# Optimization experiments

Measured on AMD Instinct MI355X. Metric: run time of the kernel, lower is better.

The kernel has to match this reference:

```python
import jax, jax.numpy as jnp
import numpy as np

H, C = 8, 32          # heads, per-head channels (h_feats)
NEG_SLOPE = 0.2


def setup_inputs() -> dict:
    key = jax.random.key(0)
    ks = jax.random.split(key, 9)
    N, E, F_IN, F_E = 50000, 800000, 128, 16
    x = jax.random.normal(ks[0], (N, F_IN), jnp.float32)
    edge_index = jax.random.randint(ks[1], (2, E), 0, N, jnp.int64)
    edge_attr = jax.random.normal(ks[2], (E, F_E), jnp.float32)
    s = 1.0 / np.sqrt(F_IN)
    W = jax.random.normal(ks[3], (H * C, F_IN), jnp.float32) * s
    W_edge = jax.random.normal(ks[4], (H * C, F_E), jnp.float32) * (1.0 / np.sqrt(F_E))
    att_src = jax.random.normal(ks[5], (H, C), jnp.float32) * (1.0 / np.sqrt(C))
    att_dst = jax.random.normal(ks[6], (H, C), jnp.float32) * (1.0 / np.sqrt(C))
    att_edge = jax.random.normal(ks[7], (H, C), jnp.float32) * (1.0 / np.sqrt(C))
    bias = jnp.zeros((C,), jnp.float32)
    return {"x": x, "edge_index": edge_index, "edge_attr": edge_attr,
            "W": W, "W_edge": W_edge, "att_src": att_src, "att_dst": att_dst,
            "att_edge": att_edge, "bias": bias}


def reference(x, edge_index, edge_attr, W, W_edge, att_src, att_dst, att_edge, bias):
    N = x.shape[0]
    src, dst = edge_index[0], edge_index[1]

    # --- add self loops, edge_attr fill_value='mean' (per-dst mean of incoming attrs) ---
    deg = jax.ops.segment_sum(jnp.ones_like(dst, dtype=edge_attr.dtype), dst, num_segments=N)
    loop_attr = jax.ops.segment_sum(edge_attr, dst, num_segments=N) / jnp.maximum(deg, 1.0)[:, None]
    loop = jnp.arange(N, dtype=src.dtype)
    src = jnp.concatenate([src, loop])
    dst = jnp.concatenate([dst, loop])
    ea = jnp.concatenate([edge_attr, loop_attr], axis=0)  # [E+N, F_e]

    # --- node projection and per-node attention terms ---
    xh = (x @ W.T).reshape(N, H, C)                      # [N,H,C]
    a_src = jnp.einsum('nhc,hc->nh', xh, att_src)        # [N,H]
    a_dst = jnp.einsum('nhc,hc->nh', xh, att_dst)        # [N,H]

    # edge attention folded: (lin_edge(e).view(E,H,C) * att_edge).sum(-1) == e @ M
    M = jnp.einsum('hcf,hc->fh', W_edge.reshape(H, C, -1), att_edge)  # [F_e,H]
    a_edge = ea @ M                                      # [E+N,H]

    alpha = a_src[src] + a_dst[dst] + a_edge             # [E+N,H]
    alpha = jnp.where(alpha >= 0, alpha, NEG_SLOPE * alpha)

    # --- scatter-softmax over edges grouped by dst node ---
    amax = jax.ops.segment_max(alpha, dst, num_segments=N)  # every node has a self loop
    ex = jnp.exp(alpha - amax[dst])
    denom = jax.ops.segment_sum(ex, dst, num_segments=N)
    att = ex / denom[dst]                                # [E+N,H]

    # --- weighted message scatter-sum ---
    msg = xh[src] * att[..., None]                       # [E+N,H,C]
    out = jax.ops.segment_sum(msg, dst, num_segments=N)  # [N,H,C]
    return out.mean(axis=1) + bias                       # concat=False -> head mean
```

## Files before the change

kernel.cpp:

```cpp
#include <hip/hip_runtime.h>
#include <math.h>

#define H 8
#define C 32
#define HC 256
#define FE 16
#define FIN 128
#define NEG_SLOPE 0.2f

__device__ __forceinline__ unsigned short f2bf(float f) {
  union { float f; unsigned int u; } a; a.f = f;
  unsigned int r = a.u;
  unsigned int lsb = (r >> 16) & 1u;
  r += 0x7fffu + lsb;
  return (unsigned short)(r >> 16);
}
__device__ __forceinline__ float bf2f(unsigned short s) {
  union { unsigned int u; float f; } a; a.u = ((unsigned int)s) << 16;
  return a.f;
}

__global__ void k_M(const float* __restrict__ W_edge, const float* __restrict__ att_edge,
                    float* __restrict__ M) {
  int t = threadIdx.x;
  int f = t >> 3, h = t & 7;
  float acc = 0.f;
#pragma unroll
  for (int c = 0; c < C; ++c)
    acc += W_edge[(h * C + c) * FE + f] * att_edge[h * C + c];
  M[f * H + h] = acc;
}

__global__ __launch_bounds__(256) void k_xh(const float* __restrict__ x,
                                            const float* __restrict__ W,
                                            const float* __restrict__ att_src,
                                            const float* __restrict__ att_dst,
                                            unsigned short* __restrict__ xhb,
                                            float* __restrict__ a_src,
                                            float* __restrict__ a_dst, int N) {
  __shared__ float As[16][132];
  __shared__ float Bs[16][132];
  int t = threadIdx.x;
  int rg = t >> 4;
  int cg = t & 15;
  int rb = blockIdx.x * 128;
  int cb = blockIdx.y * 128;
  int lr = t >> 2;
  int lk = (t & 3) * 4;

  float acc[8][8] = {};
  for (int k0 = 0; k0 < FIN; k0 += 16) {
#pragma unroll
    for (int half = 0; half < 2; ++half) {
      int row = half * 64 + lr;
      float4 va = make_float4(0.f, 0.f, 0.f, 0.f);
      if (rb + row < N) va = *(const float4*)&x[(size_t)(rb + row) * FIN + k0 + lk];
      As[lk + 0][row] = va.x; As[lk + 1][row] = va.y; As[lk + 2][row] = va.z; As[lk + 3][row] = va.w;
      float4 vb = *(const float4*)&W[(size_t)(cb + row) * FIN + k0 + lk];
      Bs[lk + 0][row] = vb.x; Bs[lk + 1][row] = vb.y; Bs[lk + 2][row] = vb.z; Bs[lk + 3][row] = vb.w;
    }
    __syncthreads();
#pragma unroll
    for (int k = 0; k < 16; ++k) {
      float4 a0 = *(const float4*)&As[k][rg * 8];
      float4 a1 = *(const float4*)&As[k][rg * 8 + 4];
      float4 b0 = *(const float4*)&Bs[k][cg * 8];
      float4 b1 = *(const float4*)&Bs[k][cg * 8 + 4];
      float av[8] = {a0.x, a0.y, a0.z, a0.w, a1.x, a1.y, a1.z, a1.w};
      float bv[8] = {b0.x, b0.y, b0.z, b0.w, b1.x, b1.y, b1.z, b1.w};
#pragma unroll
      for (int i = 0; i < 8; ++i)
#pragma unroll
        for (int j = 0; j < 8; ++j) acc[i][j] = fmaf(av[i], bv[j], acc[i][j]);
    }
    __syncthreads();
  }

  float asv[8], adv[8];
#pragma unroll
  for (int j = 0; j < 8; ++j) {
    asv[j] = att_src[cb + cg * 8 + j];
    adv[j] = att_dst[cb + cg * 8 + j];
  }
  int head = blockIdx.y * 4 + (cg >> 2);
#pragma unroll
  for (int i = 0; i < 8; ++i) {
    int r = rb + rg * 8 + i;
    if (r >= N) continue;
    unsigned int p0 = (unsigned int)f2bf(acc[i][0]) | ((unsigned int)f2bf(acc[i][1]) << 16);
    unsigned int p1 = (unsigned int)f2bf(acc[i][2]) | ((unsigned int)f2bf(acc[i][3]) << 16);
    unsigned int p2 = (unsigned int)f2bf(acc[i][4]) | ((unsigned int)f2bf(acc[i][5]) << 16);
    unsigned int p3 = (unsigned int)f2bf(acc[i][6]) | ((unsigned int)f2bf(acc[i][7]) << 16);
    uint4 pk = make_uint4(p0, p1, p2, p3);
    *(uint4*)&xhb[(size_t)r * HC + cb + cg * 8] = pk;
    float ps = 0.f, pd = 0.f;
#pragma unroll
    for (int j = 0; j < 8; ++j) { ps = fmaf(acc[i][j], asv[j], ps); pd = fmaf(acc[i][j], adv[j], pd); }
    ps += __shfl_xor(ps, 1, 64); ps += __shfl_xor(ps, 2, 64);
    pd += __shfl_xor(pd, 1, 64); pd += __shfl_xor(pd, 2, 64);
    if ((t & 3) == 0) {
      a_src[r * H + head] = ps;
      a_dst[r * H + head] = pd;
    }
  }
}

__global__ __launch_bounds__(256) void k_deg(const int* __restrict__ ei,
                                             int* __restrict__ deg, int E) {
  int e = blockIdx.x * 256 + threadIdx.x;
  if (e < E) atomicAdd(&deg[ei[E + e]], 1);
}

__global__ __launch_bounds__(256) void k_scan1(const int* __restrict__ deg,
                                               int* __restrict__ bsum, int N) {
  int t = threadIdx.x;
  int i = blockIdx.x * 256 + t;
  int v = (i < N) ? deg[i] : 0;
#pragma unroll
  for (int m = 1; m < 64; m <<= 1) v += __shfl_xor(v, m, 64);
  __shared__ int wsum[4];
  if ((t & 63) == 0) wsum[t >> 6] = v;
  __syncthreads();
  if (t == 0) bsum[blockIdx.x] = wsum[0] + wsum[1] + wsum[2] + wsum[3];
}

__global__ __launch_bounds__(256) void k_scan2(const int* __restrict__ bsum,
                                               int* __restrict__ boff, int nb) {
  __shared__ int buf[256];
  int t = threadIdx.x;
  int v = (t < nb) ? bsum[t] : 0;
  buf[t] = v;
  __syncthreads();
  for (int off = 1; off < 256; off <<= 1) {
    int y = (t >= off) ? buf[t - off] : 0;
    __syncthreads();
    buf[t] += y;
    __syncthreads();
  }
  if (t < nb) boff[t] = buf[t] - v;
}

__global__ __launch_bounds__(256) void k_scan3(const int* __restrict__ deg,
                                               const int* __restrict__ boff,
                                               int* __restrict__ rowptr,
                                               int* __restrict__ wo, int N, int E) {
  __shared__ int buf[256];
  int t = threadIdx.x;
  int i = blockIdx.x * 256 + t;
  int v = (i < N) ? deg[i] : 0;
  buf[t] = v;
  __syncthreads();
  for (int off = 1; off < 256; off <<= 1) {
    int y = (t >= off) ? buf[t - off] : 0;
    __syncthreads();
    buf[t] += y;
    __syncthreads();
  }
  if (i < N) {
    int ex = boff[blockIdx.x] + buf[t] - v;
    rowptr[i] = ex;
    wo[i] = ex;
  }
  if (i == 0) rowptr[N] = E;
}

__global__ __launch_bounds__(256) void k_edge_scatter(const int* __restrict__ ei,
                                                      const float* __restrict__ ea,
                                                      const float* __restrict__ M,
                                                      int* __restrict__ wo,
                                                      int* __restrict__ colsrc,
                                                      float* __restrict__ apre, int E) {
  __shared__ float Ms[FE * H];
  int t = threadIdx.x;
  if (t < FE * H) Ms[t] = M[t];
  __syncthreads();
  int e = blockIdx.x * 256 + t;
  if (e >= E) return;
  int s = ei[e], d = ei[E + e];
  const float4* p = (const float4*)&ea[(size_t)e * FE];
  float4 v0 = p[0], v1 = p[1], v2 = p[2], v3 = p[3];
  float eav[FE] = {v0.x, v0.y, v0.z, v0.w, v1.x, v1.y, v1.z, v1.w,
                   v2.x, v2.y, v2.z, v2.w, v3.x, v3.y, v3.z, v3.w};
  float o[H];
#pragma unroll
  for (int h = 0; h < H; ++h) {
    float acc = 0.f;
#pragma unroll
    for (int f = 0; f < FE; ++f) acc += eav[f] * Ms[f * H + h];
    o[h] = acc;
  }
  int pos = atomicAdd(&wo[d], 1);
  colsrc[pos] = s;
  float4* q = (float4*)&apre[(size_t)pos * H];
  q[0] = make_float4(o[0], o[1], o[2], o[3]);
  q[1] = make_float4(o[4], o[5], o[6], o[7]);
}

__global__ __launch_bounds__(256) void k_node(const unsigned short* __restrict__ xhb,
                                              const float* __restrict__ a_src,
                                              const float* __restrict__ a_dst,
                                              const float* __restrict__ apre,
                                              const int* __restrict__ colsrc,
                                              const int* __restrict__ rowptr,
                                              const float* __restrict__ bias,
                                              float* __restrict__ out, int N) {
  int lane = threadIdx.x & 63;
  int n = blockIdx.x * 4 + (threadIdx.x >> 6);
  if (n >= N) return;
  int start = rowptr[n];
  int deg = rowptr[n + 1] - start;
  int hc = lane >> 3;
  float adst = a_dst[n * H + hc];
  float asrc = a_src[n * H + hc];

  float m = -1e30f, l = 0.f, psum = 0.f;
  float ax = 0.f, ay = 0.f, az = 0.f, aw = 0.f;

#pragma unroll 4
  for (int j = 0; j < deg; ++j) {
    int src = colsrc[start + j];
    float ae = apre[(size_t)(start + j) * H + hc];
    psum += ae;
    float al = a_src[src * H + hc] + adst + ae;
    al = (al >= 0.f) ? al : NEG_SLOPE * al;
    float nm = fmaxf(m, al);
    float s = __expf(m - nm);
    float w = __expf(al - nm);
    m = nm;
    l = fmaf(l, s, w);
    ushort4 u = *(const ushort4*)&xhb[(size_t)src * HC + lane * 4];
    ax = fmaf(ax, s, w * bf2f(u.x));
    ay = fmaf(ay, s, w * bf2f(u.y));
    az = fmaf(az, s, w * bf2f(u.z));
    aw = fmaf(aw, s, w * bf2f(u.w));
  }

  float aself = asrc + adst + psum / fmaxf((float)deg, 1.f);
  aself = (aself >= 0.f) ? aself : NEG_SLOPE * aself;
  {
    float nm = fmaxf(m, aself);
    float s = __expf(m - nm);
    float w = __expf(aself - nm);
    m = nm;
    l = fmaf(l, s, w);
    ushort4 u = *(const ushort4*)&xhb[(size_t)n * HC + lane * 4];
    ax = fmaf(ax, s, w * bf2f(u.x));
    ay = fmaf(ay, s, w * bf2f(u.y));
    az = fmaf(az, s, w * bf2f(u.z));
    aw = fmaf(aw, s, w * bf2f(u.w));
  }
  float inv = 1.f / l;
  ax *= inv; ay *= inv; az *= inv; aw *= inv;

#pragma unroll
  for (int mm = 8; mm <= 32; mm <<= 1) {
    ax += __shfl_xor(ax, mm, 64);
    ay += __shfl_xor(ay, mm, 64);
    az += __shfl_xor(az, mm, 64);
    aw += __shfl_xor(aw, mm, 64);
  }
  if (lane < 8) {
    float4 b = ((const float4*)bias)[lane];
    float4 o;
    o.x = ax * 0.125f + b.x;
    o.y = ay * 0.125f + b.y;
    o.z = az * 0.125f + b.z;
    o.w = aw * 0.125f + b.w;
    ((float4*)&out[(size_t)n * C])[lane] = o;
  }
}

extern "C" void kernel_launch(void* const* d_in, const int* in_sizes, int n_in,
                              void* d_out, int out_size, void* d_ws, size_t ws_size,
                              hipStream_t stream) {
  const float* x        = (const float*)d_in[0];
  const int*   ei       = (const int*)d_in[1];
  const float* ea       = (const float*)d_in[2];
  const float* W        = (const float*)d_in[3];
  const float* W_edge   = (const float*)d_in[4];
  const float* att_src  = (const float*)d_in[5];
  const float* att_dst  = (const float*)d_in[6];
  const float* att_edge = (const float*)d_in[7];
  const float* bias     = (const float*)d_in[8];
  float* out = (float*)d_out;

  int N = in_sizes[0] / FIN;
  int E = in_sizes[1] / 2;
  int nb = (N + 255) / 256;

  char* ws = (char*)d_ws;
  auto take = [&](size_t bytes) {
    char* p = ws;
    ws += (bytes + 255) & ~(size_t)255;
    return p;
  };
  unsigned short* xhb = (unsigned short*)take((size_t)N * HC * 2);
  float* a_src  = (float*)take((size_t)N * H * 4);
  float* a_dst  = (float*)take((size_t)N * H * 4);
  float* apre   = (float*)take((size_t)E * H * 4);
  float* Mbuf   = (float*)take(FE * H * 4);
  int*   deg    = (int*)take((size_t)N * 4);
  int*   rowptr = (int*)take((size_t)(N + 1) * 4);
  int*   wo     = (int*)take((size_t)N * 4);
  int*   colsrc = (int*)take((size_t)E * 4);
  int*   bsum   = (int*)take((size_t)nb * 4);
  int*   boff   = (int*)take((size_t)nb * 4);

  hipMemsetAsync(deg, 0, (size_t)N * 4, stream);
  k_M<<<1, 128, 0, stream>>>(W_edge, att_edge, Mbuf);
  k_deg<<<(E + 255) / 256, 256, 0, stream>>>(ei, deg, E);
  k_xh<<<dim3((N + 127) / 128, HC / 128), 256, 0, stream>>>(x, W, att_src, att_dst, xhb, a_src, a_dst, N);
  k_scan1<<<nb, 256, 0, stream>>>(deg, bsum, N);
  k_scan2<<<1, 256, 0, stream>>>(bsum, boff, nb);
  k_scan3<<<nb, 256, 0, stream>>>(deg, boff, rowptr, wo, N, E);
  k_edge_scatter<<<(E + 255) / 256, 256, 0, stream>>>(ei, ea, Mbuf, wo, colsrc, apre, E);
  k_node<<<(N + 3) / 4, 256, 0, stream>>>(xhb, a_src, a_dst, apre, colsrc, rowptr, bias, out, N);
}
```

Before: 344.8 us.

## Use bf16 MFMA split-precision GEMM, rank-based CSR fill, bf16 edge logits

The node projection GEMM is rewritten to use MFMA 16x16x32 bf16 instructions, with the fp32 inputs split into hi/lo bf16 parts (three MFMAs per tile) to keep near-fp32 accuracy. Operands now load straight from global memory, with no LDS staging. The degree kernel records each edge's rank from its atomic, so the scatter kernel computes positions without a second round of atomics. The edge attention logits are stored as bf16 to halve that traffic, and the M matrix is computed inside the scatter kernel, which removes one launch. The costs are extra MFMA work, uncoalesced W/x loads, and precision loss in the edge logits.

```diff
diff --git a/kernel.cpp b/kernel.cpp
--- a/kernel.cpp
+++ b/kernel.cpp
@@ -8,27 +8,28 @@
 #define FIN 128
 #define NEG_SLOPE 0.2f
 
+typedef __attribute__((ext_vector_type(8))) short bf16x8;
+typedef __attribute__((ext_vector_type(4))) float f32x4;
+
 __device__ __forceinline__ unsigned short f2bf(float f) {
-  union { float f; unsigned int u; } a; a.f = f;
-  unsigned int r = a.u;
-  unsigned int lsb = (r >> 16) & 1u;
-  r += 0x7fffu + lsb;
-  return (unsigned short)(r >> 16);
+  unsigned int u = __float_as_uint(f);
+  unsigned int lsb = (u >> 16) & 1u;
+  u += 0x7fffu + lsb;
+  return (unsigned short)(u >> 16);
 }
 __device__ __forceinline__ float bf2f(unsigned short s) {
-  union { unsigned int u; float f; } a; a.u = ((unsigned int)s) << 16;
-  return a.f;
-}
-
-__global__ void k_M(const float* __restrict__ W_edge, const float* __restrict__ att_edge,
-                    float* __restrict__ M) {
-  int t = threadIdx.x;
-  int f = t >> 3, h = t & 7;
-  float acc = 0.f;
-#pragma unroll
-  for (int c = 0; c < C; ++c)
-    acc += W_edge[(h * C + c) * FE + f] * att_edge[h * C + c];
-  M[f * H + h] = acc;
+  return __uint_as_float(((unsigned int)s) << 16);
+}
+
+__device__ __forceinline__ void split8(const float* v, bf16x8& hi, bf16x8& lo) {
+#pragma unroll
+  for (int i = 0; i < 8; ++i) {
+    unsigned int u = __float_as_uint(v[i]);
+    unsigned int hu = u & 0xffff0000u;
+    float r = v[i] - __uint_as_float(hu);
+    hi[i] = (short)(hu >> 16);
+    lo[i] = (short)f2bf(r);
+  }
 }
 
 __global__ __launch_bounds__(256) void k_xh(const float* __restrict__ x,
@@ -38,77 +39,101 @@
                                             unsigned short* __restrict__ xhb,
                                             float* __restrict__ a_src,
                                             float* __restrict__ a_dst, int N) {
-  __shared__ float As[16][132];
-  __shared__ float Bs[16][132];
-  int t = threadIdx.x;
-  int rg = t >> 4;
-  int cg = t & 15;
-  int rb = blockIdx.x * 128;
-  int cb = blockIdx.y * 128;
-  int lr = t >> 2;
-  int lk = (t & 3) * 4;
-
-  float acc[8][8] = {};
-  for (int k0 = 0; k0 < FIN; k0 += 16) {
-#pragma unroll
-    for (int half = 0; half < 2; ++half) {
-      int row = half * 64 + lr;
-      float4 va = make_float4(0.f, 0.f, 0.f, 0.f);
-      if (rb + row < N) va = *(const float4*)&x[(size_t)(rb + row) * FIN + k0 + lk];
-      As[lk + 0][row] = va.x; As[lk + 1][row] = va.y; As[lk + 2][row] = va.z; As[lk + 3][row] = va.w;
-      float4 vb = *(const float4*)&W[(size_t)(cb + row) * FIN + k0 + lk];
-      Bs[lk + 0][row] = vb.x; Bs[lk + 1][row] = vb.y; Bs[lk + 2][row] = vb.z; Bs[lk + 3][row] = vb.w;
-    }
-    __syncthreads();
-#pragma unroll
-    for (int k = 0; k < 16; ++k) {
-      float4 a0 = *(const float4*)&As[k][rg * 8];
-      float4 a1 = *(const float4*)&As[k][rg * 8 + 4];
-      float4 b0 = *(const float4*)&Bs[k][cg * 8];
-      float4 b1 = *(const float4*)&Bs[k][cg * 8 + 4];
-      float av[8] = {a0.x, a0.y, a0.z, a0.w, a1.x, a1.y, a1.z, a1.w};
-      float bv[8] = {b0.x, b0.y, b0.z, b0.w, b1.x, b1.y, b1.z, b1.w};
-#pragma unroll
-      for (int i = 0; i < 8; ++i)
-#pragma unroll
-        for (int j = 0; j < 8; ++j) acc[i][j] = fmaf(av[i], bv[j], acc[i][j]);
-    }
-    __syncthreads();
-  }
-
-  float asv[8], adv[8];
-#pragma unroll
-  for (int j = 0; j < 8; ++j) {
-    asv[j] = att_src[cb + cg * 8 + j];
-    adv[j] = att_dst[cb + cg * 8 + j];
-  }
-  int head = blockIdx.y * 4 + (cg >> 2);
-#pragma unroll
-  for (int i = 0; i < 8; ++i) {
-    int r = rb + rg * 8 + i;
-    if (r >= N) continue;
-    unsigned int p0 = (unsigned int)f2bf(acc[i][0]) | ((unsigned int)f2bf(acc[i][1]) << 16);
-    unsigned int p1 = (unsigned int)f2bf(acc[i][2]) | ((unsigned int)f2bf(acc[i][3]) << 16);
-    unsigned int p2 = (unsigned int)f2bf(acc[i][4]) | ((unsigned int)f2bf(acc[i][5]) << 16);
-    unsigned int p3 = (unsigned int)f2bf(acc[i][6]) | ((unsigned int)f2bf(acc[i][7]) << 16);
-    uint4 pk = make_uint4(p0, p1, p2, p3);
-    *(uint4*)&xhb[(size_t)r * HC + cb + cg * 8] = pk;
-    float ps = 0.f, pd = 0.f;
-#pragma unroll
-    for (int j = 0; j < 8; ++j) { ps = fmaf(acc[i][j], asv[j], ps); pd = fmaf(acc[i][j], adv[j], pd); }
-    ps += __shfl_xor(ps, 1, 64); ps += __shfl_xor(ps, 2, 64);
-    pd += __shfl_xor(pd, 1, 64); pd += __shfl_xor(pd, 2, 64);
-    if ((t & 3) == 0) {
-      a_src[r * H + head] = ps;
-      a_dst[r * H + head] = pd;
+  int t = threadIdx.x;
+  int w = t >> 6, lane = t & 63;
+  int n15 = lane & 15, q = lane >> 4;
+  int nodeBase = blockIdx.x * 128 + w * 32;
+  int chBase = blockIdx.y * 128;
+
+  f32x4 acc[8][2];
+#pragma unroll
+  for (int mt = 0; mt < 8; ++mt)
+#pragma unroll
+    for (int nt = 0; nt < 2; ++nt) acc[mt][nt] = (f32x4)(0.f);
+
+  for (int ks = 0; ks < 4; ++ks) {
+    int kOff = ks * 32 + q * 8;
+    bf16x8 Bhi[2], Blo[2];
+#pragma unroll
+    for (int nt = 0; nt < 2; ++nt) {
+      int node = nodeBase + nt * 16 + n15;
+      int rn = (node < N) ? node : (N - 1);
+      const float* px = &x[(size_t)rn * FIN + kOff];
+      float vb[8];
+      *(float4*)&vb[0] = *(const float4*)px;
+      *(float4*)&vb[4] = *(const float4*)(px + 4);
+      split8(vb, Bhi[nt], Blo[nt]);
+    }
+#pragma unroll
+    for (int mt = 0; mt < 8; ++mt) {
+      const float* pw = &W[(size_t)(chBase + mt * 16 + n15) * FIN + kOff];
+      float va[8];
+      *(float4*)&va[0] = *(const float4*)pw;
+      *(float4*)&va[4] = *(const float4*)(pw + 4);
+      bf16x8 Ahi, Alo;
+      split8(va, Ahi, Alo);
+#pragma unroll
+      for (int nt = 0; nt < 2; ++nt) {
+        acc[mt][nt] = __builtin_amdgcn_mfma_f32_16x16x32_bf16(Ahi, Bhi[nt], acc[mt][nt], 0, 0, 0);
+        acc[mt][nt] = __builtin_amdgcn_mfma_f32_16x16x32_bf16(Ahi, Blo[nt], acc[mt][nt], 0, 0, 0);
+        acc[mt][nt] = __builtin_amdgcn_mfma_f32_16x16x32_bf16(Alo, Bhi[nt], acc[mt][nt], 0, 0, 0);
+      }
+    }
+  }
+
+  float ps[2][4] = {{0.f,0.f,0.f,0.f},{0.f,0.f,0.f,0.f}};
+  float pd[2][4] = {{0.f,0.f,0.f,0.f},{0.f,0.f,0.f,0.f}};
+#pragma unroll
+  for (int mt = 0; mt < 8; ++mt) {
+    int hl = mt >> 1;
+#pragma unroll
+    for (int r = 0; r < 4; ++r) {
+      int ch = chBase + mt * 16 + q * 4 + r;
+      float as_c = att_src[ch], ad_c = att_dst[ch];
+#pragma unroll
+      for (int nt = 0; nt < 2; ++nt) {
+        float val = acc[mt][nt][r];
+        ps[nt][hl] = fmaf(val, as_c, ps[nt][hl]);
+        pd[nt][hl] = fmaf(val, ad_c, pd[nt][hl]);
+      }
+    }
+#pragma unroll
+    for (int nt = 0; nt < 2; ++nt) {
+      int node = nodeBase + nt * 16 + n15;
+      if (node < N) {
+        ushort4 us;
+        us.x = f2bf(acc[mt][nt][0]); us.y = f2bf(acc[mt][nt][1]);
+        us.z = f2bf(acc[mt][nt][2]); us.w = f2bf(acc[mt][nt][3]);
+        *(ushort4*)&xhb[(size_t)node * HC + chBase + mt * 16 + q * 4] = us;
+      }
+    }
+  }
+#pragma unroll
+  for (int nt = 0; nt < 2; ++nt)
+#pragma unroll
+    for (int hl = 0; hl < 4; ++hl) {
+      ps[nt][hl] += __shfl_xor(ps[nt][hl], 16, 64);
+      ps[nt][hl] += __shfl_xor(ps[nt][hl], 32, 64);
+      pd[nt][hl] += __shfl_xor(pd[nt][hl], 16, 64);
+      pd[nt][hl] += __shfl_xor(pd[nt][hl], 32, 64);
+    }
+  if (q == 0) {
+#pragma unroll
+    for (int nt = 0; nt < 2; ++nt) {
+      int node = nodeBase + nt * 16 + n15;
+      if (node < N) {
+        *(float4*)&a_src[node * H + blockIdx.y * 4] = make_float4(ps[nt][0], ps[nt][1], ps[nt][2], ps[nt][3]);
+        *(float4*)&a_dst[node * H + blockIdx.y * 4] = make_float4(pd[nt][0], pd[nt][1], pd[nt][2], pd[nt][3]);
+      }
     }
   }
 }
 
 __global__ __launch_bounds__(256) void k_deg(const int* __restrict__ ei,
-                                             int* __restrict__ deg, int E) {
+                                             int* __restrict__ deg,
+                                             int* __restrict__ rank, int E) {
   int e = blockIdx.x * 256 + threadIdx.x;
-  if (e < E) atomicAdd(&deg[ei[E + e]], 1);
+  if (e < E) rank[e] = atomicAdd(&deg[ei[E + e]], 1);
 }
 
 __global__ __launch_bounds__(256) void k_scan1(const int* __restrict__ deg,
@@ -142,8 +167,7 @@
 
 __global__ __launch_bounds__(256) void k_scan3(const int* __restrict__ deg,
                                                const int* __restrict__ boff,
-                                               int* __restrict__ rowptr,
-                                               int* __restrict__ wo, int N, int E) {
+                                               int* __restrict__ rowptr, int N, int E) {
   __shared__ int buf[256];
   int t = threadIdx.x;
   int i = blockIdx.x * 256 + t;
@@ -156,23 +180,28 @@
     buf[t] += y;
     __syncthreads();
   }
-  if (i < N) {
-    int ex = boff[blockIdx.x] + buf[t] - v;
-    rowptr[i] = ex;
-    wo[i] = ex;
-  }
+  if (i < N) rowptr[i] = boff[blockIdx.x] + buf[t] - v;
   if (i == 0) rowptr[N] = E;
 }
 
 __global__ __launch_bounds__(256) void k_edge_scatter(const int* __restrict__ ei,
                                                       const float* __restrict__ ea,
-                                                      const float* __restrict__ M,
-                                                      int* __restrict__ wo,
+                                                      const float* __restrict__ W_edge,
+                                                      const float* __restrict__ att_edge,
+                                                      const int* __restrict__ rowptr,
+                                                      const int* __restrict__ rank,
                                                       int* __restrict__ colsrc,
-                                                      float* __restrict__ apre, int E) {
+                                                      unsigned short* __restrict__ apre16, int E) {
   __shared__ float Ms[FE * H];
   int t = threadIdx.x;
-  if (t < FE * H) Ms[t] = M[t];
+  if (t < FE * H) {
+    int f = t >> 3, h = t & 7;
+    float acc = 0.f;
+#pragma unroll
+    for (int c = 0; c < C; ++c)
+      acc += W_edge[(h * C + c) * FE + f] * att_edge[h * C + c];
+    Ms[f * H + h] = acc;
+  }
   __syncthreads();
   int e = blockIdx.x * 256 + t;
   if (e >= E) return;
@@ -189,17 +218,20 @@
     for (int f = 0; f < FE; ++f) acc += eav[f] * Ms[f * H + h];
     o[h] = acc;
   }
-  int pos = atomicAdd(&wo[d], 1);
+  int pos = rowptr[d] + rank[e];
   colsrc[pos] = s;
-  float4* q = (float4*)&apre[(size_t)pos * H];
-  q[0] = make_float4(o[0], o[1], o[2], o[3]);
-  q[1] = make_float4(o[4], o[5], o[6], o[7]);
+  uint4 pk;
+  pk.x = (unsigned int)f2bf(o[0]) | ((unsigned int)f2bf(o[1]) << 16);
+  pk.y = (unsigned int)f2bf(o[2]) | ((unsigned int)f2bf(o[3]) << 16);
+  pk.z = (unsigned int)f2bf(o[4]) | ((unsigned int)f2bf(o[5]) << 16);
+  pk.w = (unsigned int)f2bf(o[6]) | ((unsigned int)f2bf(o[7]) << 16);
+  *(uint4*)&apre16[(size_t)pos * H] = pk;
 }
 
 __global__ __launch_bounds__(256) void k_node(const unsigned short* __restrict__ xhb,
                                               const float* __restrict__ a_src,
                                               const float* __restrict__ a_dst,
-                                              const float* __restrict__ apre,
+                                              const unsigned short* __restrict__ apre16,
                                               const int* __restrict__ colsrc,
                                               const int* __restrict__ rowptr,
                                               const float* __restrict__ bias,
@@ -219,7 +251,7 @@
 #pragma unroll 4
   for (int j = 0; j < deg; ++j) {
     int src = colsrc[start + j];
-    float ae = apre[(size_t)(start + j) * H + hc];
+    float ae = bf2f(apre16[(size_t)(start + j) * H + hc]);
     psum += ae;
     float al = a_src[src * H + hc] + adst + ae;
     al = (al >= 0.f) ? al : NEG_SLOPE * al;
@@ -294,25 +326,23 @@
     ws += (bytes + 255) & ~(size_t)255;
     return p;
   };
-  unsigned short* xhb = (unsigned short*)take((size_t)N * HC * 2);
-  float* a_src  = (float*)take((size_t)N * H * 4);
-  float* a_dst  = (float*)take((size_t)N * H * 4);
-  float* apre   = (float*)take((size_t)E * H * 4);
-  float* Mbuf   = (float*)take(FE * H * 4);
-  int*   deg    = (int*)take((size_t)N * 4);
-  int*   rowptr = (int*)take((size_t)(N + 1) * 4);
-  int*   wo     = (int*)take((size_t)N * 4);
-  int*   colsrc = (int*)take((size_t)E * 4);
-  int*   bsum   = (int*)take((size_t)nb * 4);
-  int*   boff   = (int*)take((size_t)nb * 4);
+  unsigned short* xhb    = (unsigned short*)take((size_t)N * HC * 2);
+  float*          a_src  = (float*)take((size_t)N * H * 4);
+  float*          a_dst  = (float*)take((size_t)N * H * 4);
+  unsigned short* apre16 = (unsigned short*)take((size_t)E * H * 2);
+  int*            deg    = (int*)take((size_t)N * 4);
+  int*            rowptr = (int*)take((size_t)(N + 1) * 4);
+  int*            rank   = (int*)take((size_t)E * 4);
+  int*            colsrc = (int*)take((size_t)E * 4);
+  int*            bsum   = (int*)take((size_t)nb * 4);
+  int*            boff   = (int*)take((size_t)nb * 4);
 
   hipMemsetAsync(deg, 0, (size_t)N * 4, stream);
-  k_M<<<1, 128, 0, stream>>>(W_edge, att_edge, Mbuf);
-  k_deg<<<(E + 255) / 256, 256, 0, stream>>>(ei, deg, E);
-  k_xh<<<dim3((N + 127) / 128, HC / 128), 256, 0, stream>>>(x, W, att_src, att_dst, xhb, a_src, a_dst, N);
+  k_deg<<<(E + 255) / 256, 256, 0, stream>>>(ei, deg, rank, E);
+  k_xh<<<dim3((N + 127) / 128, 2), 256, 0, stream>>>(x, W, att_src, att_dst, xhb, a_src, a_dst, N);
   k_scan1<<<nb, 256, 0, stream>>>(deg, bsum, N);
   k_scan2<<<1, 256, 0, stream>>>(bsum, boff, nb);
-  k_scan3<<<nb, 256, 0, stream>>>(deg, boff, rowptr, wo, N, E);
-  k_edge_scatter<<<(E + 255) / 256, 256, 0, stream>>>(ei, ea, Mbuf, wo, colsrc, apre, E);
-  k_node<<<(N + 3) / 4, 256, 0, stream>>>(xhb, a_src, a_dst, apre, colsrc, rowptr, bias, out, N);
-}
+  k_scan3<<<nb, 256, 0, stream>>>(deg, boff, rowptr, N, E);
+  k_edge_scatter<<<(E + 255) / 256, 256, 0, stream>>>(ei, ea, W_edge, att_edge, rowptr, rank, colsrc, apre16, E);
+  k_node<<<(N + 3) / 4, 256, 0, stream>>>(xhb, a_src, a_dst, apre16, colsrc, rowptr, bias, out, N);
+}
```

After: 313.0 us. 9.2% less time.
